# Performance work log

Measured on AMD Instinct MI355X. Metric: run time of the kernel, lower is better.

Reference implementation:

```python
import jax, jax.numpy as jnp
import numpy as np

N_NODES = 100000
N_EDGES = 1600000
D_IN = 64
D_OUT = 64


def setup_inputs() -> dict:
    key = jax.random.key(0)
    ks = jax.random.split(key, 8)
    x = jax.random.normal(ks[0], (N_NODES, D_IN), dtype=jnp.float32)
    edge_rows = jax.random.randint(ks[1], (N_EDGES,), 0, N_NODES, dtype=jnp.int32)
    edge_cols = jax.random.randint(ks[2], (N_EDGES,), 0, N_NODES, dtype=jnp.int32)
    edge_vals = jax.random.uniform(ks[3], (N_EDGES,), dtype=jnp.float32)
    # xavier_uniform with gain=2.0: limit = gain * sqrt(6 / (fan_in + fan_out))
    lim = 2.0 * float(np.sqrt(6.0 / (D_IN + D_OUT)))
    weight_own = jax.random.uniform(ks[4], (D_IN, D_OUT), jnp.float32, -lim, lim)
    weight_nbr = jax.random.uniform(ks[5], (D_IN, D_OUT), jnp.float32, -lim, lim)
    weight_temp = jax.random.uniform(ks[6], (D_IN, D_OUT), jnp.float32, -lim, lim)
    bias = jnp.zeros((D_OUT,), jnp.float32)
    return {
        "x": x,
        "edge_rows": edge_rows,
        "edge_cols": edge_cols,
        "edge_vals": edge_vals,
        "weight_own": weight_own,
        "weight_nbr": weight_nbr,
        "weight_temp": weight_temp,
        "bias": bias,
    }


def _spmm(edge_rows, edge_cols, edge_vals, dense):
    # COO sparse [N,N] @ dense [N,D]: gather source rows, scale by edge value,
    # scatter-add into destination rows.
    msgs = edge_vals[:, None] * dense[edge_cols]  # [E, D]
    return jax.ops.segment_sum(msgs, edge_rows, num_segments=N_NODES)


def reference(x, edge_rows, edge_cols, edge_vals, weight_own, weight_nbr, weight_temp, bias):
    support = x @ weight_own    # [N, D_OUT]
    support1 = x @ weight_nbr
    support2 = x @ weight_temp
    output = _spmm(edge_rows, edge_cols, edge_vals, support)
    output1 = _spmm(edge_rows, edge_cols, edge_vals, support1)
    output2 = _spmm(edge_rows, edge_cols, edge_vals, support2)
    return output + output1 + output2 + bias
```

## Files before the change

### kernel.cpp

```cpp
#include <hip/hip_runtime.h>
#include <hip/hip_bf16.h>

#define D 64
#define RPB 256
#define RSH 8
#define NBMAX 1024
#define CPAD 16

__global__ __launch_bounds__(256) void gemm_kernel(const float* __restrict__ x,
                                                   const float* __restrict__ w0,
                                                   const float* __restrict__ w1,
                                                   const float* __restrict__ w2,
                                                   __hip_bfloat16* __restrict__ support,
                                                   int n) {
    __shared__ float Ws[D * D];
    __shared__ float xs[4][D];

    for (int i = threadIdx.x; i < D * D; i += 256)
        Ws[i] = w0[i] + w1[i] + w2[i];
    __syncthreads();

    const int wid  = threadIdx.x >> 6;
    const int lane = threadIdx.x & 63;
    int row = blockIdx.x * 4 + wid;
    const int nw = gridDim.x * 4;

    for (; row < n; row += nw) {
        xs[wid][lane] = x[(size_t)row * D + lane];
        float acc = 0.0f;
#pragma unroll
        for (int k = 0; k < D; ++k) {
            acc += xs[wid][k] * Ws[k * D + lane];
        }
        support[(size_t)row * D + lane] = __float2bfloat16(acc);
    }
}

__global__ __launch_bounds__(256) void gemm_f32_kernel(const float* __restrict__ x,
                                                       const float* __restrict__ w0,
                                                       const float* __restrict__ w1,
                                                       const float* __restrict__ w2,
                                                       float* __restrict__ support,
                                                       int n) {
    __shared__ float Ws[D * D];
    __shared__ float xs[4][D];
    for (int i = threadIdx.x; i < D * D; i += 256)
        Ws[i] = w0[i] + w1[i] + w2[i];
    __syncthreads();
    const int wid  = threadIdx.x >> 6;
    const int lane = threadIdx.x & 63;
    int row = blockIdx.x * 4 + wid;
    const int nw = gridDim.x * 4;
    for (; row < n; row += nw) {
        xs[wid][lane] = x[(size_t)row * D + lane];
        float acc = 0.0f;
#pragma unroll
        for (int k = 0; k < D; ++k) acc += xs[wid][k] * Ws[k * D + lane];
        support[(size_t)row * D + lane] = acc;
    }
}

__global__ __launch_bounds__(256) void bucket_hist_kernel(const int* __restrict__ rows,
                                                          int ne, int* __restrict__ gcnt,
                                                          int nb) {
    __shared__ int lcnt[NBMAX];
    for (int i = threadIdx.x; i < nb; i += 256) lcnt[i] = 0;
    __syncthreads();
    int i = blockIdx.x * 256 + threadIdx.x;
    int stride = gridDim.x * 256;
    for (; i < ne; i += stride) atomicAdd(&lcnt[rows[i] >> RSH], 1);
    __syncthreads();
    for (int b = threadIdx.x; b < nb; b += 256) {
        int c = lcnt[b];
        if (c) atomicAdd(&gcnt[b * CPAD], c);
    }
}

__global__ __launch_bounds__(256) void bucket_scan_kernel(const int* __restrict__ gcnt,
                                                          int nb,
                                                          int* __restrict__ base,
                                                          int* __restrict__ cursor) {
    __shared__ int ts[256];
    const int tid = threadIdx.x;
    int b0 = tid * 4;
    int v[4]; int tsum = 0;
#pragma unroll
    for (int j = 0; j < 4; ++j) {
        int idx = b0 + j;
        v[j] = (idx < nb) ? gcnt[idx * CPAD] : 0;
        tsum += v[j];
    }
    ts[tid] = tsum;
    __syncthreads();
    for (int off = 1; off < 256; off <<= 1) {
        int t = (tid >= off) ? ts[tid - off] : 0;
        __syncthreads();
        ts[tid] += t;
        __syncthreads();
    }
    int excl = ts[tid] - tsum;
#pragma unroll
    for (int j = 0; j < 4; ++j) {
        int idx = b0 + j;
        if (idx < nb) { base[idx] = excl; cursor[idx * CPAD] = excl; }
        excl += v[j];
    }
    if (tid == 255) base[nb] = excl;
}

__global__ __launch_bounds__(256) void bin_scatter_kernel(const int* __restrict__ rows,
                                                          const int* __restrict__ cols,
                                                          const float* __restrict__ vals,
                                                          int ne,
                                                          int* __restrict__ cursor,
                                                          int nb,
                                                          int2* __restrict__ binned) {
    __shared__ int lcnt[NBMAX];
    __shared__ int lbase[NBMAX];
    const int tid = threadIdx.x;
    const int ce = (ne + gridDim.x - 1) / gridDim.x;
    const int e0 = blockIdx.x * ce;
    const int e1 = min(ne, e0 + ce);

    for (int i = tid; i < nb; i += 256) lcnt[i] = 0;
    __syncthreads();
    for (int e = e0 + tid; e < e1; e += 256) atomicAdd(&lcnt[rows[e] >> RSH], 1);
    __syncthreads();
    for (int b = tid; b < nb; b += 256) {
        int c = lcnt[b];
        lbase[b] = c ? atomicAdd(&cursor[b * CPAD], c) : 0;
    }
    __syncthreads();
    for (int i = tid; i < nb; i += 256) lcnt[i] = 0;
    __syncthreads();
    for (int e = e0 + tid; e < e1; e += 256) {
        int r = rows[e];
        int b = r >> RSH;
        int loc = atomicAdd(&lcnt[b], 1);
        int2 cv;
        cv.x = ((r & (RPB - 1)) << 17) | cols[e];
        cv.y = __float_as_int(vals[e]);
        binned[lbase[b] + loc] = cv;
    }
}

__global__ __launch_bounds__(1024) void local_csr_kernel(const int* __restrict__ base,
                                                         const int2* __restrict__ binned,
                                                         int* __restrict__ rowptr,
                                                         int2* __restrict__ csr,
                                                         int n) {
    __shared__ int lh[RPB];
    __shared__ int lp[RPB];
    const int tid = threadIdx.x;
    const int b = blockIdx.x;
    const int jb = base[b], je = base[b + 1];

    for (int i = tid; i < RPB; i += 1024) lh[i] = 0;
    __syncthreads();
    for (int j = jb + tid; j < je; j += 1024) atomicAdd(&lh[binned[j].x >> 17], 1);
    __syncthreads();
    if (tid < RPB) lp[tid] = lh[tid];
    __syncthreads();
    for (int off = 1; off < RPB; off <<= 1) {
        int t = (tid < RPB && tid >= off) ? lp[tid - off] : 0;
        __syncthreads();
        if (tid < RPB) lp[tid] += t;
        __syncthreads();
    }
    if (tid < RPB) {
        int excl = lp[tid] - lh[tid];
        int start = jb + excl;
        lh[tid] = start;
        int r = b * RPB + tid;
        if (r < n) rowptr[r] = start;
    }
    __syncthreads();
    for (int j = jb + tid; j < je; j += 1024) {
        int2 e = binned[j];
        int rl = e.x >> 17;
        int pos = atomicAdd(&lh[rl], 1);
        int2 o; o.x = e.x & 0x1FFFF; o.y = e.y;
        csr[pos] = o;
    }
}

__global__ __launch_bounds__(256) void pull2_kernel(const int* __restrict__ rowptr,
                                                    const int2* __restrict__ csr,
                                                    const unsigned int* __restrict__ sup32,
                                                    const float* __restrict__ bias,
                                                    float* __restrict__ out, int n) {
    const int tid  = threadIdx.x;
    const int lane = tid & 63;
    const int half = lane >> 5;
    const int sub  = lane & 31;
    const int wave = blockIdx.x * 4 + (tid >> 6);
    const int nwave = gridDim.x * 4;
    const float2 b2 = reinterpret_cast<const float2*>(bias)[sub];

    for (int w = wave; 2 * w < n; w += nwave) {
        const int r = 2 * w + half;
        float ax = 0.0f, ay = 0.0f;
        if (r < n) {
            const int jb = rowptr[r], je = rowptr[r + 1];
            int j = jb;
            for (; j + 7 < je; j += 8) {
                int2 e[8];
#pragma unroll
                for (int u = 0; u < 8; ++u) e[u] = csr[j + u];
                unsigned int g[8];
#pragma unroll
                for (int u = 0; u < 8; ++u)
                    g[u] = sup32[(size_t)e[u].x * 32 + sub];
#pragma unroll
                for (int u = 0; u < 8; ++u) {
                    float v = __int_as_float(e[u].y);
                    ax += v * __uint_as_float(g[u] << 16);
                    ay += v * __uint_as_float(g[u] & 0xffff0000u);
                }
            }
            for (; j + 1 < je; j += 2) {
                int2 e0 = csr[j], e1 = csr[j + 1];
                unsigned int u0 = sup32[(size_t)e0.x * 32 + sub];
                unsigned int u1 = sup32[(size_t)e1.x * 32 + sub];
                float v0 = __int_as_float(e0.y), v1 = __int_as_float(e1.y);
                ax += v0 * __uint_as_float(u0 << 16);
                ay += v0 * __uint_as_float(u0 & 0xffff0000u);
                ax += v1 * __uint_as_float(u1 << 16);
                ay += v1 * __uint_as_float(u1 & 0xffff0000u);
            }
            if (j < je) {
                int2 e = csr[j];
                unsigned int u = sup32[(size_t)e.x * 32 + sub];
                float v = __int_as_float(e.y);
                ax += v * __uint_as_float(u << 16);
                ay += v * __uint_as_float(u & 0xffff0000u);
            }
            float2 o; o.x = ax + b2.x; o.y = ay + b2.y;
            reinterpret_cast<float2*>(out)[(size_t)r * 32 + sub] = o;
        }
    }
}

__global__ __launch_bounds__(256) void init_kernel(const float* __restrict__ bias,
                                                   float* __restrict__ out, int total4) {
    int i = blockIdx.x * 256 + threadIdx.x;
    int stride = gridDim.x * 256;
    for (; i < total4; i += stride) {
        int base4 = (i * 4) & (D - 1);
        float4 bv;
        bv.x = bias[base4 + 0]; bv.y = bias[base4 + 1];
        bv.z = bias[base4 + 2]; bv.w = bias[base4 + 3];
        reinterpret_cast<float4*>(out)[i] = bv;
    }
}

__global__ __launch_bounds__(256) void scatter_kernel(const int* __restrict__ rows,
                                                      const int* __restrict__ cols,
                                                      const float* __restrict__ vals,
                                                      const float* __restrict__ support,
                                                      float* __restrict__ out, int ne) {
    const int wid  = blockIdx.x * 4 + (threadIdx.x >> 6);
    const int lane = threadIdx.x & 63;
    const int nw = gridDim.x * 4;
    for (int e = wid; e < ne; e += nw) {
        const int r = rows[e];
        const int c = cols[e];
        const float v = vals[e];
        unsafeAtomicAdd(&out[(size_t)r * D + lane], v * support[(size_t)c * D + lane]);
    }
}

extern "C" void kernel_launch(void* const* d_in, const int* in_sizes, int n_in,
                              void* d_out, int out_size, void* d_ws, size_t ws_size,
                              hipStream_t stream) {
    const float* x         = (const float*)d_in[0];
    const int*   edge_rows = (const int*)d_in[1];
    const int*   edge_cols = (const int*)d_in[2];
    const float* edge_vals = (const float*)d_in[3];
    const float* w_own     = (const float*)d_in[4];
    const float* w_nbr     = (const float*)d_in[5];
    const float* w_temp    = (const float*)d_in[6];
    const float* bias      = (const float*)d_in[7];

    float* out = (float*)d_out;
    const int n_nodes = in_sizes[0] / D;
    const int n_edges = in_sizes[1];
    const int nb = (n_nodes + RPB - 1) / RPB;

    char* ws = (char*)d_ws;
    size_t off = 0;
    auto take = [&](size_t bytes) -> char* {
        char* p = ws + off;
        off = (off + bytes + 15) & ~(size_t)15;
        return p;
    };
    __hip_bfloat16* support = (__hip_bfloat16*)take((size_t)n_nodes * D * sizeof(__hip_bfloat16));
    int2* binned = (int2*)take((size_t)n_edges * sizeof(int2));
    int2* csr    = (int2*)take((size_t)n_edges * sizeof(int2));
    int*  rowptr = (int*) take((size_t)(n_nodes + 1) * sizeof(int));
    int*  gcnt   = (int*) take((size_t)nb * CPAD * sizeof(int));
    int*  base   = (int*) take((size_t)(nb + 1) * sizeof(int));
    int*  cursor = (int*) take((size_t)nb * CPAD * sizeof(int));
    const bool full_fits = (off <= ws_size) && (nb <= NBMAX) && (n_nodes <= (1 << 17));

    if (full_fits) {
        gemm_kernel<<<1024, 256, 0, stream>>>(x, w_own, w_nbr, w_temp, support, n_nodes);
        hipMemsetAsync(gcnt, 0, (size_t)nb * CPAD * sizeof(int), stream);
        bucket_hist_kernel<<<1024, 256, 0, stream>>>(edge_rows, n_edges, gcnt, nb);
        bucket_scan_kernel<<<1, 256, 0, stream>>>(gcnt, nb, base, cursor);
        bin_scatter_kernel<<<512, 256, 0, stream>>>(edge_rows, edge_cols, edge_vals,
                                                    n_edges, cursor, nb, binned);
        local_csr_kernel<<<nb, 1024, 0, stream>>>(base, binned, rowptr, csr, n_nodes);
        hipMemcpyAsync(rowptr + n_nodes, base + nb, sizeof(int),
                       hipMemcpyDeviceToDevice, stream);
        pull2_kernel<<<2048, 256, 0, stream>>>(rowptr, csr, (const unsigned int*)support,
                                               bias, out, n_nodes);
    } else {
        float* support_f = (float*)d_ws;
        gemm_f32_kernel<<<1024, 256, 0, stream>>>(x, w_own, w_nbr, w_temp, support_f, n_nodes);
        int total4 = (n_nodes * D) / 4;
        int blocks = (total4 + 255) / 256; if (blocks > 2048) blocks = 2048;
        init_kernel<<<blocks, 256, 0, stream>>>(bias, out, total4);
        scatter_kernel<<<2048, 256, 0, stream>>>(edge_rows, edge_cols, edge_vals,
                                                 support_f, out, n_edges);
    }
}
```

Baseline: 145.8 us.

## Coarsen edge buckets to 1024 rows and split local CSR build four ways

Each bucket now covers 1024 rows instead of 256, so there are far fewer buckets. The bucket scan becomes one element per thread, and the binning scatter writes longer contiguous runs per bucket. The local CSR build now launches four 512-thread blocks per bucket. Each block recomputes the full bucket histogram and prefix sum, then places only the edges whose rows fall in its quarter. This keeps block count and parallelism up, at the cost of reading each bucket's binned edges four times.

```diff
diff --git a/kernel.cpp b/kernel.cpp
--- a/kernel.cpp
+++ b/kernel.cpp
@@ -2,9 +2,9 @@
 #include <hip/hip_bf16.h>
 
 #define D 64
-#define RPB 256
-#define RSH 8
-#define NBMAX 1024
+#define RPB 1024
+#define RSH 10
+#define NBB 128
 #define CPAD 16
 
 __global__ __launch_bounds__(256) void gemm_kernel(const float* __restrict__ x,
@@ -63,7 +63,7 @@
 __global__ __launch_bounds__(256) void bucket_hist_kernel(const int* __restrict__ rows,
                                                           int ne, int* __restrict__ gcnt,
                                                           int nb) {
-    __shared__ int lcnt[NBMAX];
+    __shared__ int lcnt[NBB];
     for (int i = threadIdx.x; i < nb; i += 256) lcnt[i] = 0;
     __syncthreads();
     int i = blockIdx.x * 256 + threadIdx.x;
@@ -82,15 +82,8 @@
                                                           int* __restrict__ cursor) {
     __shared__ int ts[256];
     const int tid = threadIdx.x;
-    int b0 = tid * 4;
-    int v[4]; int tsum = 0;
-#pragma unroll
-    for (int j = 0; j < 4; ++j) {
-        int idx = b0 + j;
-        v[j] = (idx < nb) ? gcnt[idx * CPAD] : 0;
-        tsum += v[j];
-    }
-    ts[tid] = tsum;
+    int v = (tid < nb) ? gcnt[tid * CPAD] : 0;
+    ts[tid] = v;
     __syncthreads();
     for (int off = 1; off < 256; off <<= 1) {
         int t = (tid >= off) ? ts[tid - off] : 0;
@@ -98,14 +91,9 @@
         ts[tid] += t;
         __syncthreads();
     }
-    int excl = ts[tid] - tsum;
-#pragma unroll
-    for (int j = 0; j < 4; ++j) {
-        int idx = b0 + j;
-        if (idx < nb) { base[idx] = excl; cursor[idx * CPAD] = excl; }
-        excl += v[j];
-    }
-    if (tid == 255) base[nb] = excl;
+    int excl = ts[tid] - v;
+    if (tid < nb) { base[tid] = excl; cursor[tid * CPAD] = excl; }
+    if (tid == 255) base[nb] = ts[255];
 }
 
 __global__ __launch_bounds__(256) void bin_scatter_kernel(const int* __restrict__ rows,
@@ -115,8 +103,8 @@
                                                           int* __restrict__ cursor,
                                                           int nb,
                                                           int2* __restrict__ binned) {
-    __shared__ int lcnt[NBMAX];
-    __shared__ int lbase[NBMAX];
+    __shared__ int lcnt[NBB];
+    __shared__ int lbase[NBB];
     const int tid = threadIdx.x;
     const int ce = (ne + gridDim.x - 1) / gridDim.x;
     const int e0 = blockIdx.x * ce;
@@ -144,43 +132,52 @@
     }
 }
 
-__global__ __launch_bounds__(1024) void local_csr_kernel(const int* __restrict__ base,
-                                                         const int2* __restrict__ binned,
-                                                         int* __restrict__ rowptr,
-                                                         int2* __restrict__ csr,
-                                                         int n) {
+__global__ __launch_bounds__(512) void local_csr_kernel(const int* __restrict__ base,
+                                                        const int2* __restrict__ binned,
+                                                        int* __restrict__ rowptr,
+                                                        int2* __restrict__ csr,
+                                                        int n) {
     __shared__ int lh[RPB];
-    __shared__ int lp[RPB];
+    __shared__ int ts[512];
     const int tid = threadIdx.x;
-    const int b = blockIdx.x;
+    const int b = blockIdx.x >> 2;
+    const int q = blockIdx.x & 3;
     const int jb = base[b], je = base[b + 1];
 
-    for (int i = tid; i < RPB; i += 1024) lh[i] = 0;
-    __syncthreads();
-    for (int j = jb + tid; j < je; j += 1024) atomicAdd(&lh[binned[j].x >> 17], 1);
-    __syncthreads();
-    if (tid < RPB) lp[tid] = lh[tid];
-    __syncthreads();
-    for (int off = 1; off < RPB; off <<= 1) {
-        int t = (tid < RPB && tid >= off) ? lp[tid - off] : 0;
+    lh[2 * tid] = 0; lh[2 * tid + 1] = 0;
+    __syncthreads();
+    for (int j = jb + tid; j < je; j += 512)
+        atomicAdd(&lh[binned[j].x >> 17], 1);
+    __syncthreads();
+
+    const int v0 = lh[2 * tid], v1 = lh[2 * tid + 1];
+    const int tsum = v0 + v1;
+    ts[tid] = tsum;
+    __syncthreads();
+    for (int off = 1; off < 512; off <<= 1) {
+        int t = (tid >= off) ? ts[tid - off] : 0;
         __syncthreads();
-        if (tid < RPB) lp[tid] += t;
+        ts[tid] += t;
         __syncthreads();
     }
-    if (tid < RPB) {
-        int excl = lp[tid] - lh[tid];
-        int start = jb + excl;
-        lh[tid] = start;
-        int r = b * RPB + tid;
-        if (r < n) rowptr[r] = start;
-    }
-    __syncthreads();
-    for (int j = jb + tid; j < je; j += 1024) {
+    int excl = ts[tid] - tsum + jb;
+    __syncthreads();
+
+    const int r0 = b * RPB + 2 * tid;
+    lh[2 * tid] = excl;
+    if (r0 < n) rowptr[r0] = excl;
+    lh[2 * tid + 1] = excl + v0;
+    if (r0 + 1 < n) rowptr[r0 + 1] = excl + v0;
+    __syncthreads();
+
+    for (int j = jb + tid; j < je; j += 512) {
         int2 e = binned[j];
         int rl = e.x >> 17;
-        int pos = atomicAdd(&lh[rl], 1);
-        int2 o; o.x = e.x & 0x1FFFF; o.y = e.y;
-        csr[pos] = o;
+        if ((rl >> 8) == q) {
+            int pos = atomicAdd(&lh[rl], 1);
+            int2 o; o.x = e.x & 0x1FFFF; o.y = e.y;
+            csr[pos] = o;
+        }
     }
 }
 
@@ -301,16 +298,16 @@
     int*  gcnt   = (int*) take((size_t)nb * CPAD * sizeof(int));
     int*  base   = (int*) take((size_t)(nb + 1) * sizeof(int));
     int*  cursor = (int*) take((size_t)nb * CPAD * sizeof(int));
-    const bool full_fits = (off <= ws_size) && (nb <= NBMAX) && (n_nodes <= (1 << 17));
+    const bool full_fits = (off <= ws_size) && (nb <= NBB) && (n_nodes <= (1 << 17));
 
     if (full_fits) {
         gemm_kernel<<<1024, 256, 0, stream>>>(x, w_own, w_nbr, w_temp, support, n_nodes);
         hipMemsetAsync(gcnt, 0, (size_t)nb * CPAD * sizeof(int), stream);
-        bucket_hist_kernel<<<1024, 256, 0, stream>>>(edge_rows, n_edges, gcnt, nb);
+        bucket_hist_kernel<<<512, 256, 0, stream>>>(edge_rows, n_edges, gcnt, nb);
         bucket_scan_kernel<<<1, 256, 0, stream>>>(gcnt, nb, base, cursor);
         bin_scatter_kernel<<<512, 256, 0, stream>>>(edge_rows, edge_cols, edge_vals,
                                                     n_edges, cursor, nb, binned);
-        local_csr_kernel<<<nb, 1024, 0, stream>>>(base, binned, rowptr, csr, n_nodes);
+        local_csr_kernel<<<nb * 4, 512, 0, stream>>>(base, binned, rowptr, csr, n_nodes);
         hipMemcpyAsync(rowptr + n_nodes, base + nb, sizeof(int),
                        hipMemcpyDeviceToDevice, stream);
         pull2_kernel<<<2048, 256, 0, stream>>>(rowptr, csr, (const unsigned int*)support,
```

Result: faster. 139.7 us (-4.2%).
